# Kernel optimization log

Measured on AMD Instinct MI355X. Metric: run time of the kernel, lower is better.

## Reference

```python
import jax, jax.numpy as jnp
import numpy as np

B, T, D, H = 16384, 80, 12, 128


def setup_inputs() -> dict:
    key = jax.random.key(0)
    ks = jax.random.split(key, 20)
    stdv = lambda n: 1.0 / np.sqrt(n)
    u = lambda k, shp, s: jax.random.uniform(k, shp, jnp.float32, -s, s)
    inp = {
        'values': jax.random.normal(ks[0], (B, T, D), jnp.float32),
        'masks': (jax.random.uniform(ks[1], (B, T, D)) < 0.8).astype(jnp.float32),
        'deltas': jax.random.uniform(ks[2], (B, T, D), jnp.float32, 0.0, 5.0),
        'td_h_W': u(ks[3], (H, D), stdv(H)), 'td_h_b': u(ks[4], (H,), stdv(H)),
        'td_x_W': u(ks[5], (D, D), stdv(D)), 'td_x_b': u(ks[6], (D,), stdv(D)),
        'hist_W': u(ks[7], (D, H), stdv(H)), 'hist_b': u(ks[8], (D,), stdv(H)),
        'feat_W': u(ks[9], (D, D), stdv(D)), 'feat_b': u(ks[10], (D,), stdv(D)),
        'wc_W': u(ks[11], (D, 2 * D), stdv(2 * D)), 'wc_b': u(ks[12], (D,), stdv(2 * D)),
        'W_ih': u(ks[13], (4 * H, 2 * D), stdv(H)), 'b_ih': u(ks[14], (4 * H,), stdv(H)),
        'W_hh': u(ks[15], (4 * H, H), stdv(H)), 'b_hh': u(ks[16], (4 * H,), stdv(H)),
        'out_W': u(ks[17], (1, H), stdv(H)), 'out_b': u(ks[18], (1,), stdv(H)),
    }
    return inp


def _forward(values, masks, deltas, td_h_W, td_h_b, td_x_W, td_x_b,
             hist_W, hist_b, feat_W, feat_b, wc_W, wc_b,
             W_ih, b_ih, W_hh, b_hh, out_W, out_b):
    eye = jnp.eye(D, dtype=values.dtype)
    td_x_Wd = td_x_W * eye            # diagonal temporal decay
    feat_Wm = feat_W * (1.0 - eye)

    xs = (jnp.swapaxes(values, 0, 1),  # [T,B,D]
          jnp.swapaxes(masks, 0, 1),
          jnp.swapaxes(deltas, 0, 1))

    def step(carry, xmd):
        h, c, x_loss = carry
        x, m, d = xmd
        gamma_h = jnp.exp(-jax.nn.relu(d @ td_h_W.T + td_h_b))   # [B,H]
        gamma_x = jnp.exp(-jax.nn.relu(d @ td_x_Wd.T + td_x_b))  # [B,D]
        h = h * gamma_h
        x_h = h @ hist_W.T + hist_b
        denom = jnp.sum(m) + 1e-5
        x_loss += jnp.sum(jnp.abs(x - x_h) * m) / denom
        x_c = m * x + (1.0 - m) * x_h
        z_h = x_c @ feat_Wm.T + feat_b
        x_loss += jnp.sum(jnp.abs(x - z_h) * m) / denom
        alpha = jnp.concatenate([gamma_x, m], axis=1) @ wc_W.T + wc_b
        c_h = alpha * z_h + (1.0 - alpha) * x_h
        x_loss += jnp.sum(jnp.abs(x - c_h) * m) / denom
        c_c = m * x + (1.0 - m) * c_h
        inp = jnp.concatenate([c_c, m], axis=1)                  # [B,2D]
        gates = inp @ W_ih.T + b_ih + h @ W_hh.T + b_hh          # [B,4H]
        i, f, g, o = jnp.split(gates, 4, axis=1)
        c = jax.nn.sigmoid(f) * c + jax.nn.sigmoid(i) * jnp.tanh(g)
        h = jax.nn.sigmoid(o) * jnp.tanh(c)
        return (h, c, x_loss), c_c

    h0 = jnp.zeros((values.shape[0], H), values.dtype)
    c0 = jnp.zeros((values.shape[0], H), values.dtype)
    (h, c, x_loss), imps = jax.lax.scan(step, (h0, c0, jnp.float32(0.0)), xs)
    loss = x_loss / T
    predictions = jax.nn.sigmoid(h @ out_W.T + out_b)            # [B,1]
    imputations = jnp.swapaxes(imps, 0, 1)                       # [B,T,D]
    return loss, predictions, imputations


def reference(values, masks, deltas, td_h_W, td_h_b, td_x_W, td_x_b,
              hist_W, hist_b, feat_W, feat_b, wc_W, wc_b,
              W_ih, b_ih, W_hh, b_hh, out_W, out_b):
    return _forward(values, masks, deltas, td_h_W, td_h_b, td_x_W, td_x_b,
                    hist_W, hist_b, feat_W, feat_b, wc_W, wc_b,
                    W_ih, b_ih, W_hh, b_hh, out_W, out_b)
```

## Files before the change

### kernel.cpp

```cpp
#include <hip/hip_runtime.h>

#define B_ 16384
#define T_ 80
#define D_ 12
#define H_ 128
#define BT 32
#define NTH 512
#define NBLK (B_ / BT)

#define NLOG2E -1.4426950408889634f
#define TWOLOG2E 2.8853900817779268f

typedef unsigned short us_t;
typedef unsigned int u32_t;
typedef short bf16x8 __attribute__((ext_vector_type(8)));
typedef float f32x4 __attribute__((ext_vector_type(4)));

__device__ __forceinline__ us_t f2bf(float f){
  u32_t x = __float_as_uint(f);
  return (us_t)((x + 0x7FFFu + ((x >> 16) & 1u)) >> 16);
}
__device__ __forceinline__ float bf2f(us_t u){
  union { u32_t i; float f; } v; v.i = ((u32_t)u) << 16; return v.f;
}
__device__ __forceinline__ float rcpf(float x){ return __builtin_amdgcn_rcpf(x); }
#if __has_builtin(__builtin_amdgcn_exp2f)
__device__ __forceinline__ float exp2f_(float x){ return __builtin_amdgcn_exp2f(x); }
#else
__device__ __forceinline__ float exp2f_(float x){ return __expf(0.6931471805599453f * x); }
#endif
__device__ __forceinline__ float sigm(float x){ return rcpf(1.f + __expf(-x)); }

__global__ void k_denom(const float* __restrict__ masks, float* __restrict__ denomInv) {
  int t = blockIdx.x, tid = threadIdx.x;
  float s = 0.f;
  for (int b = tid; b < B_; b += 256) {
    const float4* p = (const float4*)(masks + ((size_t)b * T_ + t) * D_);
    float4 a = p[0], c = p[1], d = p[2];
    s += a.x + a.y + a.z + a.w + c.x + c.y + c.z + c.w + d.x + d.y + d.z + d.w;
  }
  __shared__ float r[256];
  r[tid] = s; __syncthreads();
  for (int st = 128; st > 0; st >>= 1) { if (tid < st) r[tid] += r[tid + st]; __syncthreads(); }
  if (tid == 0) denomInv[t] = 1.f / (r[0] + 1e-5f);
}

__global__ void k_pack(const float* __restrict__ W_ih, const float* __restrict__ W_hh,
                       const float* __restrict__ hist_W, const float* __restrict__ td_h_W,
                       const float* __restrict__ b_ih, const float* __restrict__ b_hh,
                       us_t* __restrict__ Wb, us_t* __restrict__ histB,
                       us_t* __restrict__ tdhwB, float* __restrict__ bias_pk) {
  int idx = blockIdx.x * 256 + threadIdx.x;
  if (idx < 81920) {
    int i = idx & 7, lane = (idx >> 3) & 63, rest = idx >> 9;
    int kc = rest % 5; rest /= 5;
    int g = rest & 3, w = rest >> 2;
    int n = g * 128 + w * 16 + (lane & 15);
    int k = kc * 32 + ((lane >> 4) << 3) + i;
    float v = 0.f;
    if (k < 24) v = W_ih[n * 24 + k];
    else if (k < 152) v = W_hh[n * 128 + (k - 24)];
    float s = (g == 2) ? TWOLOG2E : NLOG2E;
    Wb[idx] = f2bf(v * s);
  } else if (idx < 83968) {
    int e = idx - 81920;
    int i = e & 7, lane = (e >> 3) & 63, kc = e >> 9;
    int col = lane & 15, k = kc * 32 + ((lane >> 4) << 3) + i;
    histB[e] = f2bf(col < 12 ? hist_W[col * 128 + k] : 0.f);
  } else if (idx < 88064) {
    int e = idx - 83968;
    int i = e & 7, lane = (e >> 3) & 63, w = e >> 9;
    int n = w * 16 + (lane & 15), k = ((lane >> 4) << 3) + i;
    tdhwB[e] = f2bf(k < 12 ? td_h_W[n * 12 + k] * NLOG2E : 0.f);
  } else if (idx < 88576) {
    int e = idx - 88064;
    int g = e >> 7;
    float s = (g == 2) ? TWOLOG2E : NLOG2E;
    bias_pk[e] = (b_ih[e] + b_hh[e]) * s;
  }
}

#define STAGE_WRITE(BUF, V) do { \
  if (la == 0) { \
    x_s[BUF][lb][lq*4+0] = (V).x; x_s[BUF][lb][lq*4+1] = (V).y; \
    x_s[BUF][lb][lq*4+2] = (V).z; x_s[BUF][lb][lq*4+3] = (V).w; \
  } else if (la == 1) { \
    m_s[BUF][lb][lq*4+0] = (V).x; m_s[BUF][lb][lq*4+1] = (V).y; \
    m_s[BUF][lb][lq*4+2] = (V).z; m_s[BUF][lb][lq*4+3] = (V).w; \
    float _mv0=(V).x,_mv1=(V).y,_mv2=(V).z,_mv3=(V).w; \
    int _k = 12 + lq*4; \
    A_s[BUF][(_k+0)>>3][lb][(_k+0)&7] = f2bf(_mv0); \
    A_s[BUF][(_k+1)>>3][lb][(_k+1)&7] = f2bf(_mv1); \
    A_s[BUF][(_k+2)>>3][lb][(_k+2)&7] = f2bf(_mv2); \
    A_s[BUF][(_k+3)>>3][lb][(_k+3)&7] = f2bf(_mv3); \
  } else { \
    float _dv[4] = {(V).x,(V).y,(V).z,(V).w}; \
    _Pragma("unroll") \
    for (int _j = 0; _j < 4; ++_j) { \
      int _i = lq*4+_j; \
      gx_s[BUF][lb][_i] = exp2f_(fminf(fmaf(_dv[_j], tdxd_s[_i], tdxb_s[_i]), 0.f)); \
      dA_s[_i>>3][lb][_i&7] = f2bf(_dv[_j]); \
    } \
  } \
} while(0)

__global__ __launch_bounds__(NTH) void k_main(
    const float* __restrict__ values, const float* __restrict__ masks, const float* __restrict__ deltas,
    const float* __restrict__ td_h_b, const float* __restrict__ td_x_W, const float* __restrict__ td_x_b,
    const float* __restrict__ hist_b, const float* __restrict__ feat_W, const float* __restrict__ feat_b,
    const float* __restrict__ wc_W, const float* __restrict__ wc_b,
    const float* __restrict__ out_W, const float* __restrict__ out_b,
    const float* __restrict__ denomInv, const float* __restrict__ bias_pk,
    const us_t* __restrict__ Wb, const us_t* __restrict__ histB, const us_t* __restrict__ tdhwB,
    float* __restrict__ blockLoss, float* __restrict__ out_pred, float* __restrict__ out_imp) {

  __shared__ __align__(16) us_t A_s[2][20][BT][8];
  __shared__ __align__(16) us_t dA_s[4][BT][8];
  __shared__ __align__(16) us_t histB_s[4][64][8];
  __shared__ float x_s[2][BT][13], m_s[2][BT][13], gx_s[2][BT][13];
  __shared__ float cct_s[BT][13], xh_s[BT][13], al_s[BT][13];
  __shared__ float featW_s[12][12], wcW_s[12][24];
  __shared__ float featb_s[12], wcb_s[12], tdxd_s[12], tdxb_s[12];
  __shared__ float outW_s[128];
  __shared__ float outb_s;
  __shared__ float red_s[NTH];

  const int tid = threadIdx.x;
  const int bs = blockIdx.x * BT;
  const int w = tid >> 6, l = tid & 63;
  const int lr = l & 15, lg = l >> 4;

  for (int i = tid; i < 144; i += NTH)
    featW_s[i / 12][i % 12] = ((i / 12) == (i % 12)) ? 0.f : feat_W[i];
  for (int i = tid; i < 288; i += NTH) ((float*)wcW_s)[i] = wc_W[i];
  if (tid < 12) {
    featb_s[tid] = feat_b[tid]; wcb_s[tid] = wc_b[tid];
    tdxd_s[tid] = td_x_W[tid * 12 + tid] * NLOG2E;
    tdxb_s[tid] = td_x_b[tid] * NLOG2E;
  }
  if (tid < 128) outW_s[tid] = out_W[tid];
  if (tid == 0) outb_s = out_b[0];
  for (int i = tid; i < 2 * 20 * BT * 8; i += NTH) ((us_t*)A_s)[i] = 0;
  for (int i = tid; i < 4 * BT * 8; i += NTH) ((us_t*)dA_s)[i] = 0;
  for (int i = tid; i < 2048; i += NTH) ((us_t*)histB_s)[i] = histB[i];

  bf16x8 bq[4][5];
  #pragma unroll
  for (int g = 0; g < 4; ++g)
    #pragma unroll
    for (int kc = 0; kc < 5; ++kc)
      bq[g][kc] = *(const bf16x8*)(Wb + (size_t)((((w * 4 + g) * 5 + kc) * 64 + l) << 3));
  const bf16x8 twf = *(const bf16x8*)(tdhwB + (size_t)(((w * 64) + l) << 3));
  float bjs[4];
  #pragma unroll
  for (int g = 0; g < 4; ++g) bjs[g] = bias_pk[g * 128 + w * 16 + lr];
  const float tdhb_j = td_h_b[w * 16 + lr] * NLOG2E;
  const float hbias = hist_b[lr < 12 ? lr : 0];

  const int lt = tid - 128;
  const bool isLoader = (lt >= 0 && lt < 288);
  const int la = isLoader ? lt / 96 : 0;
  const int lrm = isLoader ? lt % 96 : 0;
  const int lb = lrm / 3, lq = lrm % 3;
  const float* lsrc = (la == 0) ? values : (la == 1) ? masks : deltas;

  float c_st[2][4] = {{0.f,0.f,0.f,0.f},{0.f,0.f,0.f,0.f}};
  float lossAcc = 0.f;
  int cur = 0;
  __syncthreads();

  if (isLoader) {
    float4 pv = *(const float4*)(lsrc + ((size_t)(bs + lb) * T_) * D_ + lq * 4);
    STAGE_WRITE(0, pv);
  }
  __syncthreads();

  for (int t = 0; t < T_; ++t) {
    const float dInv = denomInv[t];
    const int nxt = cur ^ 1;
    float4 ldv;

    if (w < 2) {
      f32x4 xacc = {0.f, 0.f, 0.f, 0.f};
      #pragma unroll
      for (int kc = 0; kc < 4; ++kc) {
        const bf16x8 af = *(const bf16x8*)&A_s[cur][3 + kc * 4 + lg][w * 16 + lr][0];
        const bf16x8 hf = *(const bf16x8*)&histB_s[kc][l][0];
        xacc = __builtin_amdgcn_mfma_f32_16x16x32_bf16(af, hf, xacc, 0, 0, 0);
      }
      if (lr < 12) {
        #pragma unroll
        for (int r = 0; r < 4; ++r) xh_s[w * 16 + lg * 4 + r][lr] = xacc[r] + hbias;
      }
    } else {
      if (isLoader) {
        if (t + 1 < T_)
          ldv = *(const float4*)(lsrc + ((size_t)(bs + lb) * T_ + (t + 1)) * D_ + lq * 4);
      } else if (t > 0) {
        int ib = (tid - 416) / 3, iq = (tid - 416) % 3;
        float4 v = make_float4(cct_s[ib][iq * 4 + 0], cct_s[ib][iq * 4 + 1],
                               cct_s[ib][iq * 4 + 2], cct_s[ib][iq * 4 + 3]);
        *(float4*)(out_imp + ((size_t)(bs + ib) * T_ + (t - 1)) * D_ + iq * 4) = v;
      }
      int ai = tid - 128, b = ai & 31, i = ai >> 5;
      float al = wcb_s[i];
      #pragma unroll
      for (int k = 0; k < 12; ++k) {
        al = fmaf(gx_s[cur][b][k], wcW_s[i][k], al);
        al = fmaf(m_s[cur][b][k], wcW_s[i][12 + k], al);
      }
      al_s[b][i] = al;
    }
    __syncthreads();

    if (isLoader && (t + 1 < T_)) STAGE_WRITE(nxt, ldv);
    if (tid < 384) {
      int b = tid & 31, i = tid >> 5;
      float xh = xh_s[b][i], xv = x_s[cur][b][i], mv = m_s[cur][b][i];
      float es = fabsf(xv - xh) * mv;
      float zh = featb_s[i];
      #pragma unroll
      for (int k = 0; k < 12; ++k) {
        float xck = fmaf(m_s[cur][b][k], x_s[cur][b][k] - xh_s[b][k], xh_s[b][k]);
        zh = fmaf(xck, featW_s[i][k], zh);
      }
      es += fabsf(xv - zh) * mv;
      float al = al_s[b][i];
      float ch = fmaf(al, zh - xh, xh);
      es += fabsf(xv - ch) * mv;
      lossAcc = fmaf(es, dInv, lossAcc);
      float cc = fmaf(mv, xv - ch, ch);
      cct_s[b][i] = cc;
      A_s[cur][i >> 3][b][i & 7] = f2bf(cc);
    }
    __syncthreads();

    {
      f32x4 acc[2][4];
      #pragma unroll
      for (int m = 0; m < 2; ++m)
        #pragma unroll
        for (int g = 0; g < 4; ++g)
          acc[m][g] = (f32x4){bjs[g], bjs[g], bjs[g], bjs[g]};
      #pragma unroll
      for (int kc = 0; kc < 5; ++kc) {
        const bf16x8 a0 = *(const bf16x8*)&A_s[cur][kc * 4 + lg][lr][0];
        const bf16x8 a1 = *(const bf16x8*)&A_s[cur][kc * 4 + lg][16 + lr][0];
        #pragma unroll
        for (int g = 0; g < 4; ++g) {
          acc[0][g] = __builtin_amdgcn_mfma_f32_16x16x32_bf16(a0, bq[g][kc], acc[0][g], 0, 0, 0);
          acc[1][g] = __builtin_amdgcn_mfma_f32_16x16x32_bf16(a1, bq[g][kc], acc[1][g], 0, 0, 0);
        }
      }
      f32x4 g0 = {tdhb_j, tdhb_j, tdhb_j, tdhb_j};
      f32x4 g1 = g0;
      const bf16x8 d0 = *(const bf16x8*)&dA_s[lg][lr][0];
      const bf16x8 d1 = *(const bf16x8*)&dA_s[lg][16 + lr][0];
      g0 = __builtin_amdgcn_mfma_f32_16x16x32_bf16(d0, twf, g0, 0, 0, 0);
      g1 = __builtin_amdgcn_mfma_f32_16x16x32_bf16(d1, twf, g1, 0, 0, 0);
      const bool dec = (t + 1 < T_);
      const int kgh = 3 + 2 * w + (lr >> 3), pgh = lr & 7;
      #pragma unroll
      for (int m = 0; m < 2; ++m) {
        #pragma unroll
        for (int r = 0; r < 4; ++r) {
          float gi = rcpf(1.f + exp2f_(acc[m][0][r]));
          float gf = rcpf(1.f + exp2f_(acc[m][1][r]));
          float gg = 1.f - 2.f * rcpf(1.f + exp2f_(acc[m][2][r]));
          float go = rcpf(1.f + exp2f_(acc[m][3][r]));
          float c = fmaf(gf, c_st[m][r], gi * gg);
          c_st[m][r] = c;
          float th = 1.f - 2.f * rcpf(1.f + exp2f_(TWOLOG2E * c));
          float pre = (m == 0 ? g0[r] : g1[r]);
          float gh = dec ? exp2f_(fminf(pre, 0.f)) : 1.f;
          A_s[nxt][kgh][m * 16 + lg * 4 + r][pgh] = f2bf(go * th * gh);
        }
      }
    }
    __syncthreads();
    cur = nxt;
  }

  if (tid >= 416) {
    int ib = (tid - 416) / 3, iq = (tid - 416) % 3;
    float4 v = make_float4(cct_s[ib][iq * 4 + 0], cct_s[ib][iq * 4 + 1],
                           cct_s[ib][iq * 4 + 2], cct_s[ib][iq * 4 + 3]);
    *(float4*)(out_imp + ((size_t)(bs + ib) * T_ + (T_ - 1)) * D_ + iq * 4) = v;
  }

  if (tid < BT) {
    float a = outb_s;
    #pragma unroll 4
    for (int k = 0; k < H_; ++k)
      a = fmaf(bf2f(A_s[cur][3 + (k >> 3)][tid][k & 7]), outW_s[k], a);
    out_pred[bs + tid] = sigm(a);
  }

  red_s[tid] = lossAcc;
  __syncthreads();
  for (int s = NTH / 2; s > 0; s >>= 1) { if (tid < s) red_s[tid] += red_s[tid + s]; __syncthreads(); }
  if (tid == 0) blockLoss[blockIdx.x] = red_s[0];
}

__global__ void k_final(const float* __restrict__ blockLoss, float* __restrict__ out_loss) {
  __shared__ float r[256];
  int tid = threadIdx.x;
  r[tid] = blockLoss[tid] + blockLoss[tid + 256];
  __syncthreads();
  for (int s = 128; s > 0; s >>= 1) { if (tid < s) r[tid] += r[tid + s]; __syncthreads(); }
  if (tid == 0) out_loss[0] = r[0] * (1.f / (float)T_);
}

extern "C" void kernel_launch(void* const* d_in, const int* in_sizes, int n_in,
                              void* d_out, int out_size, void* d_ws, size_t ws_size,
                              hipStream_t stream) {
  const float* values = (const float*)d_in[0];
  const float* masks  = (const float*)d_in[1];
  const float* deltas = (const float*)d_in[2];
  const float* td_h_W = (const float*)d_in[3];
  const float* td_h_b = (const float*)d_in[4];
  const float* td_x_W = (const float*)d_in[5];
  const float* td_x_b = (const float*)d_in[6];
  const float* hist_W = (const float*)d_in[7];
  const float* hist_b = (const float*)d_in[8];
  const float* feat_W = (const float*)d_in[9];
  const float* feat_b = (const float*)d_in[10];
  const float* wc_W   = (const float*)d_in[11];
  const float* wc_b   = (const float*)d_in[12];
  const float* W_ih   = (const float*)d_in[13];
  const float* b_ih   = (const float*)d_in[14];
  const float* W_hh   = (const float*)d_in[15];
  const float* b_hh   = (const float*)d_in[16];
  const float* out_W  = (const float*)d_in[17];
  const float* out_b  = (const float*)d_in[18];

  float* ws_f      = (float*)d_ws;
  float* denomInv  = ws_f;
  float* bias_pk   = ws_f + 128;
  float* blockLoss = ws_f + 1024;
  us_t* Wb    = (us_t*)(ws_f + 2048);
  us_t* histB = Wb + 81920;
  us_t* tdhwB = histB + 2048;

  float* out_f = (float*)d_out;

  k_denom<<<T_, 256, 0, stream>>>(masks, denomInv);
  k_pack<<<346, 256, 0, stream>>>(W_ih, W_hh, hist_W, td_h_W, b_ih, b_hh,
                                  Wb, histB, tdhwB, bias_pk);
  k_main<<<NBLK, NTH, 0, stream>>>(values, masks, deltas, td_h_b, td_x_W, td_x_b,
                                   hist_b, feat_W, feat_b, wc_W, wc_b,
                                   out_W, out_b, denomInv, bias_pk, Wb, histB, tdhwB,
                                   blockLoss, out_f + 1, out_f + 1 + B_);
  k_final<<<1, 256, 0, stream>>>(blockLoss, out_f);
}
```

Baseline: 492.2 us.

## Compute alpha gate via MFMA and rebalance warp roles in recurrent kernel

Replaces the scalar 24-term alpha (wc) projection, which 384 threads computed from shared memory, with a single wave doing two bf16 MFMAs against a prepacked wc_W fragment. The gamma_x and mask inputs are now staged directly as bf16 in a new shared tile. Warp roles shift so loaders start later and one wave writes each imputation row with three float4 stores. It also adds a hardware bf16 pack instruction for on-device conversions and raises wave priority around the LSTM MFMA section. Alpha now carries bf16 rounding of its inputs and weights, which may perturb accuracy.

```diff
diff --git a/kernel.cpp b/kernel.cpp
--- a/kernel.cpp
+++ b/kernel.cpp
@@ -16,9 +16,14 @@
 typedef short bf16x8 __attribute__((ext_vector_type(8)));
 typedef float f32x4 __attribute__((ext_vector_type(4)));
 
-__device__ __forceinline__ us_t f2bf(float f){
+__device__ __forceinline__ us_t f2bf_bit(float f){
   u32_t x = __float_as_uint(f);
   return (us_t)((x + 0x7FFFu + ((x >> 16) & 1u)) >> 16);
+}
+__device__ __forceinline__ us_t f2bf(float f){
+  u32_t r;
+  asm("v_cvt_pk_bf16_f32 %0, %1, %2" : "=v"(r) : "v"(f), "v"(f));
+  return (us_t)r;
 }
 __device__ __forceinline__ float bf2f(us_t u){
   union { u32_t i; float f; } v; v.i = ((u32_t)u) << 16; return v.f;
@@ -48,8 +53,10 @@
 __global__ void k_pack(const float* __restrict__ W_ih, const float* __restrict__ W_hh,
                        const float* __restrict__ hist_W, const float* __restrict__ td_h_W,
                        const float* __restrict__ b_ih, const float* __restrict__ b_hh,
+                       const float* __restrict__ wc_W,
                        us_t* __restrict__ Wb, us_t* __restrict__ histB,
-                       us_t* __restrict__ tdhwB, float* __restrict__ bias_pk) {
+                       us_t* __restrict__ tdhwB, float* __restrict__ bias_pk,
+                       us_t* __restrict__ wcB) {
   int idx = blockIdx.x * 256 + threadIdx.x;
   if (idx < 81920) {
     int i = idx & 7, lane = (idx >> 3) & 63, rest = idx >> 9;
@@ -61,22 +68,27 @@
     if (k < 24) v = W_ih[n * 24 + k];
     else if (k < 152) v = W_hh[n * 128 + (k - 24)];
     float s = (g == 2) ? TWOLOG2E : NLOG2E;
-    Wb[idx] = f2bf(v * s);
+    Wb[idx] = f2bf_bit(v * s);
   } else if (idx < 83968) {
     int e = idx - 81920;
     int i = e & 7, lane = (e >> 3) & 63, kc = e >> 9;
     int col = lane & 15, k = kc * 32 + ((lane >> 4) << 3) + i;
-    histB[e] = f2bf(col < 12 ? hist_W[col * 128 + k] : 0.f);
+    histB[e] = f2bf_bit(col < 12 ? hist_W[col * 128 + k] : 0.f);
   } else if (idx < 88064) {
     int e = idx - 83968;
     int i = e & 7, lane = (e >> 3) & 63, w = e >> 9;
     int n = w * 16 + (lane & 15), k = ((lane >> 4) << 3) + i;
-    tdhwB[e] = f2bf(k < 12 ? td_h_W[n * 12 + k] * NLOG2E : 0.f);
+    tdhwB[e] = f2bf_bit(k < 12 ? td_h_W[n * 12 + k] * NLOG2E : 0.f);
   } else if (idx < 88576) {
     int e = idx - 88064;
     int g = e >> 7;
     float s = (g == 2) ? TWOLOG2E : NLOG2E;
     bias_pk[e] = (b_ih[e] + b_hh[e]) * s;
+  } else if (idx < 89088) {
+    int e = idx - 88576;
+    int i = e & 7, lane = e >> 3;
+    int col = lane & 15, k = ((lane >> 4) << 3) + i;
+    wcB[e] = f2bf_bit((col < 12 && k < 24) ? wc_W[col * 24 + k] : 0.f);
   }
 }
 
@@ -87,18 +99,21 @@
   } else if (la == 1) { \
     m_s[BUF][lb][lq*4+0] = (V).x; m_s[BUF][lb][lq*4+1] = (V).y; \
     m_s[BUF][lb][lq*4+2] = (V).z; m_s[BUF][lb][lq*4+3] = (V).w; \
-    float _mv0=(V).x,_mv1=(V).y,_mv2=(V).z,_mv3=(V).w; \
-    int _k = 12 + lq*4; \
-    A_s[BUF][(_k+0)>>3][lb][(_k+0)&7] = f2bf(_mv0); \
-    A_s[BUF][(_k+1)>>3][lb][(_k+1)&7] = f2bf(_mv1); \
-    A_s[BUF][(_k+2)>>3][lb][(_k+2)&7] = f2bf(_mv2); \
-    A_s[BUF][(_k+3)>>3][lb][(_k+3)&7] = f2bf(_mv3); \
+    float _mv[4] = {(V).x,(V).y,(V).z,(V).w}; \
+    _Pragma("unroll") \
+    for (int _j = 0; _j < 4; ++_j) { \
+      int _k = 12 + lq*4 + _j; \
+      us_t _mb = f2bf(_mv[_j]); \
+      A_s[BUF][_k>>3][lb][_k&7] = _mb; \
+      aA_s[_k>>3][lb][_k&7] = _mb; \
+    } \
   } else { \
     float _dv[4] = {(V).x,(V).y,(V).z,(V).w}; \
     _Pragma("unroll") \
     for (int _j = 0; _j < 4; ++_j) { \
       int _i = lq*4+_j; \
-      gx_s[BUF][lb][_i] = exp2f_(fminf(fmaf(_dv[_j], tdxd_s[_i], tdxb_s[_i]), 0.f)); \
+      float _gx = exp2f_(fminf(fmaf(_dv[_j], tdxd_s[_i], tdxb_s[_i]), 0.f)); \
+      aA_s[_i>>3][lb][_i&7] = f2bf(_gx); \
       dA_s[_i>>3][lb][_i&7] = f2bf(_dv[_j]); \
     } \
   } \
@@ -108,19 +123,21 @@
     const float* __restrict__ values, const float* __restrict__ masks, const float* __restrict__ deltas,
     const float* __restrict__ td_h_b, const float* __restrict__ td_x_W, const float* __restrict__ td_x_b,
     const float* __restrict__ hist_b, const float* __restrict__ feat_W, const float* __restrict__ feat_b,
-    const float* __restrict__ wc_W, const float* __restrict__ wc_b,
+    const float* __restrict__ wc_b,
     const float* __restrict__ out_W, const float* __restrict__ out_b,
     const float* __restrict__ denomInv, const float* __restrict__ bias_pk,
     const us_t* __restrict__ Wb, const us_t* __restrict__ histB, const us_t* __restrict__ tdhwB,
+    const us_t* __restrict__ wcB,
     float* __restrict__ blockLoss, float* __restrict__ out_pred, float* __restrict__ out_imp) {
 
   __shared__ __align__(16) us_t A_s[2][20][BT][8];
   __shared__ __align__(16) us_t dA_s[4][BT][8];
+  __shared__ __align__(16) us_t aA_s[4][BT][8];
   __shared__ __align__(16) us_t histB_s[4][64][8];
-  __shared__ float x_s[2][BT][13], m_s[2][BT][13], gx_s[2][BT][13];
+  __shared__ float x_s[2][BT][13], m_s[2][BT][13];
   __shared__ float cct_s[BT][13], xh_s[BT][13], al_s[BT][13];
-  __shared__ float featW_s[12][12], wcW_s[12][24];
-  __shared__ float featb_s[12], wcb_s[12], tdxd_s[12], tdxb_s[12];
+  __shared__ float featW_s[12][12];
+  __shared__ float featb_s[12], tdxd_s[12], tdxb_s[12];
   __shared__ float outW_s[128];
   __shared__ float outb_s;
   __shared__ float red_s[NTH];
@@ -132,16 +149,15 @@
 
   for (int i = tid; i < 144; i += NTH)
     featW_s[i / 12][i % 12] = ((i / 12) == (i % 12)) ? 0.f : feat_W[i];
-  for (int i = tid; i < 288; i += NTH) ((float*)wcW_s)[i] = wc_W[i];
   if (tid < 12) {
-    featb_s[tid] = feat_b[tid]; wcb_s[tid] = wc_b[tid];
+    featb_s[tid] = feat_b[tid];
     tdxd_s[tid] = td_x_W[tid * 12 + tid] * NLOG2E;
     tdxb_s[tid] = td_x_b[tid] * NLOG2E;
   }
   if (tid < 128) outW_s[tid] = out_W[tid];
   if (tid == 0) outb_s = out_b[0];
   for (int i = tid; i < 2 * 20 * BT * 8; i += NTH) ((us_t*)A_s)[i] = 0;
-  for (int i = tid; i < 4 * BT * 8; i += NTH) ((us_t*)dA_s)[i] = 0;
+  for (int i = tid; i < 4 * BT * 8; i += NTH) { ((us_t*)dA_s)[i] = 0; ((us_t*)aA_s)[i] = 0; }
   for (int i = tid; i < 2048; i += NTH) ((us_t*)histB_s)[i] = histB[i];
 
   bf16x8 bq[4][5];
@@ -151,13 +167,15 @@
     for (int kc = 0; kc < 5; ++kc)
       bq[g][kc] = *(const bf16x8*)(Wb + (size_t)((((w * 4 + g) * 5 + kc) * 64 + l) << 3));
   const bf16x8 twf = *(const bf16x8*)(tdhwB + (size_t)(((w * 64) + l) << 3));
+  const bf16x8 wcf = *(const bf16x8*)(wcB + (size_t)(l << 3));
   float bjs[4];
   #pragma unroll
   for (int g = 0; g < 4; ++g) bjs[g] = bias_pk[g * 128 + w * 16 + lr];
   const float tdhb_j = td_h_b[w * 16 + lr] * NLOG2E;
   const float hbias = hist_b[lr < 12 ? lr : 0];
-
-  const int lt = tid - 128;
+  const float wcb_lr = (lr < 12) ? wc_b[lr] : 0.f;
+
+  const int lt = tid - 192;
   const bool isLoader = (lt >= 0 && lt < 288);
   const int la = isLoader ? lt / 96 : 0;
   const int lrm = isLoader ? lt % 96 : 0;
@@ -192,24 +210,31 @@
         #pragma unroll
         for (int r = 0; r < 4; ++r) xh_s[w * 16 + lg * 4 + r][lr] = xacc[r] + hbias;
       }
-    } else {
-      if (isLoader) {
-        if (t + 1 < T_)
-          ldv = *(const float4*)(lsrc + ((size_t)(bs + lb) * T_ + (t + 1)) * D_ + lq * 4);
-      } else if (t > 0) {
-        int ib = (tid - 416) / 3, iq = (tid - 416) % 3;
-        float4 v = make_float4(cct_s[ib][iq * 4 + 0], cct_s[ib][iq * 4 + 1],
-                               cct_s[ib][iq * 4 + 2], cct_s[ib][iq * 4 + 3]);
-        *(float4*)(out_imp + ((size_t)(bs + ib) * T_ + (t - 1)) * D_ + iq * 4) = v;
-      }
-      int ai = tid - 128, b = ai & 31, i = ai >> 5;
-      float al = wcb_s[i];
-      #pragma unroll
-      for (int k = 0; k < 12; ++k) {
-        al = fmaf(gx_s[cur][b][k], wcW_s[i][k], al);
-        al = fmaf(m_s[cur][b][k], wcW_s[i][12 + k], al);
-      }
-      al_s[b][i] = al;
+    } else if (w == 2) {
+      f32x4 ac0 = {wcb_lr, wcb_lr, wcb_lr, wcb_lr};
+      f32x4 ac1 = ac0;
+      const bf16x8 a0 = *(const bf16x8*)&aA_s[lg][lr][0];
+      const bf16x8 a1 = *(const bf16x8*)&aA_s[lg][16 + lr][0];
+      ac0 = __builtin_amdgcn_mfma_f32_16x16x32_bf16(a0, wcf, ac0, 0, 0, 0);
+      ac1 = __builtin_amdgcn_mfma_f32_16x16x32_bf16(a1, wcf, ac1, 0, 0, 0);
+      if (lr < 12) {
+        #pragma unroll
+        for (int r = 0; r < 4; ++r) {
+          al_s[lg * 4 + r][lr] = ac0[r];
+          al_s[16 + lg * 4 + r][lr] = ac1[r];
+        }
+      }
+    } else if (isLoader) {
+      if (t + 1 < T_)
+        ldv = *(const float4*)(lsrc + ((size_t)(bs + lb) * T_ + (t + 1)) * D_ + lq * 4);
+    } else if (t > 0) {
+      int ib = tid - 480;
+      #pragma unroll
+      for (int q = 0; q < 3; ++q) {
+        float4 v = make_float4(cct_s[ib][q * 4 + 0], cct_s[ib][q * 4 + 1],
+                               cct_s[ib][q * 4 + 2], cct_s[ib][q * 4 + 3]);
+        *(float4*)(out_imp + ((size_t)(bs + ib) * T_ + (t - 1)) * D_ + q * 4) = v;
+      }
     }
     __syncthreads();
 
@@ -242,6 +267,7 @@
         #pragma unroll
         for (int g = 0; g < 4; ++g)
           acc[m][g] = (f32x4){bjs[g], bjs[g], bjs[g], bjs[g]};
+      __builtin_amdgcn_s_setprio(1);
       #pragma unroll
       for (int kc = 0; kc < 5; ++kc) {
         const bf16x8 a0 = *(const bf16x8*)&A_s[cur][kc * 4 + lg][lr][0];
@@ -258,6 +284,7 @@
       const bf16x8 d1 = *(const bf16x8*)&dA_s[lg][16 + lr][0];
       g0 = __builtin_amdgcn_mfma_f32_16x16x32_bf16(d0, twf, g0, 0, 0, 0);
       g1 = __builtin_amdgcn_mfma_f32_16x16x32_bf16(d1, twf, g1, 0, 0, 0);
+      __builtin_amdgcn_s_setprio(0);
       const bool dec = (t + 1 < T_);
       const int kgh = 3 + 2 * w + (lr >> 3), pgh = lr & 7;
       #pragma unroll
@@ -281,11 +308,14 @@
     cur = nxt;
   }
 
-  if (tid >= 416) {
-    int ib = (tid - 416) / 3, iq = (tid - 416) % 3;
-    float4 v = make_float4(cct_s[ib][iq * 4 + 0], cct_s[ib][iq * 4 + 1],
-                           cct_s[ib][iq * 4 + 2], cct_s[ib][iq * 4 + 3]);
-    *(float4*)(out_imp + ((size_t)(bs + ib) * T_ + (T_ - 1)) * D_ + iq * 4) = v;
+  if (tid >= 480) {
+    int ib = tid - 480;
+    #pragma unroll
+    for (int q = 0; q < 3; ++q) {
+      float4 v = make_float4(cct_s[ib][q * 4 + 0], cct_s[ib][q * 4 + 1],
+                             cct_s[ib][q * 4 + 2], cct_s[ib][q * 4 + 3]);
+      *(float4*)(out_imp + ((size_t)(bs + ib) * T_ + (T_ - 1)) * D_ + q * 4) = v;
+    }
   }
 
   if (tid < BT) {
@@ -341,15 +371,16 @@
   us_t* Wb    = (us_t*)(ws_f + 2048);
   us_t* histB = Wb + 81920;
   us_t* tdhwB = histB + 2048;
+  us_t* wcB   = tdhwB + 4096;
 
   float* out_f = (float*)d_out;
 
   k_denom<<<T_, 256, 0, stream>>>(masks, denomInv);
-  k_pack<<<346, 256, 0, stream>>>(W_ih, W_hh, hist_W, td_h_W, b_ih, b_hh,
-                                  Wb, histB, tdhwB, bias_pk);
+  k_pack<<<348, 256, 0, stream>>>(W_ih, W_hh, hist_W, td_h_W, b_ih, b_hh, wc_W,
+                                  Wb, histB, tdhwB, bias_pk, wcB);
   k_main<<<NBLK, NTH, 0, stream>>>(values, masks, deltas, td_h_b, td_x_W, td_x_b,
-                                   hist_b, feat_W, feat_b, wc_W, wc_b,
-                                   out_W, out_b, denomInv, bias_pk, Wb, histB, tdhwB,
+                                   hist_b, feat_W, feat_b, wc_b,
+                                   out_W, out_b, denomInv, bias_pk, Wb, histB, tdhwB, wcB,
                                    blockLoss, out_f + 1, out_f + 1 + B_);
   k_final<<<1, 256, 0, stream>>>(blockLoss, out_f);
 }
```

Measured after the change: 457.5 us. 7.0% less time.
